# Optimization experiments

Measured on AMD Instinct MI355X. Metric: run time of the kernel, lower is better.

Reference implementation:

```python
import jax, jax.numpy as jnp
import numpy as np

B, T, D, K = 4, 2048, 1024, 4

def setup_inputs() -> dict:
    key = jax.random.key(0)
    ks = jax.random.split(key, 4)
    u = jax.random.normal(ks[0], (B, T, D), dtype=jnp.float32)
    s0 = jnp.zeros((B, K, D), dtype=jnp.float32)
    W_in = jax.random.normal(ks[1], (K * D, D), dtype=jnp.float32) * (1.0 / np.sqrt(D))
    b_in = jnp.zeros((K * D,), dtype=jnp.float32)
    W_out = jax.random.normal(ks[2], (D, K * D), dtype=jnp.float32) * (1.0 / np.sqrt(K * D))
    b_out = jnp.zeros((D,), dtype=jnp.float32)
    decay_logit = jax.random.normal(ks[3], (K,), dtype=jnp.float32)
    return {"u": u, "s0": s0, "W_in": W_in, "b_in": b_in,
            "W_out": W_out, "b_out": b_out, "decay_logit": decay_logit}

def reference(u, s0, W_in, b_in, W_out, b_out, decay_logit):
    # u: (B,T,D); s0: (B,K,D)
    Bb, Tt, Dd = u.shape
    Kk = decay_logit.shape[0]
    # input projection -> (B,T,K,D) -> (T,B,K,D) for scan over time
    inp = (jnp.einsum('btd,ed->bte', u, W_in) + b_in).reshape(Bb, Tt, Kk, Dd)
    xs = jnp.transpose(inp, (1, 0, 2, 3))  # (T,B,K,D)
    decay = jax.nn.sigmoid(decay_logit).reshape(1, Kk, 1)  # (1,K,1)

    def step(s, x):
        s_next = decay * s + x
        return s_next, s_next

    s_last, s_seq = jax.lax.scan(step, s0, xs)  # s_seq: (T,B,K,D)
    g_in = jnp.transpose(s_seq, (1, 0, 2, 3)).reshape(Bb, Tt, Kk * Dd)
    g = jnp.einsum('bte,de->btd', g_in, W_out) + b_out
    return g, s_last
```

## Files before the change

kernel.cpp:

```cpp
#include <hip/hip_runtime.h>


#define Bb 4
#define Tt 2048
#define Dd 1024
#define Kk 4
#define BT (Bb*Tt)
#define Ee (Kk*Dd)
#define NCH 32
#define LCH 64

typedef __bf16 bf16x8 __attribute__((ext_vector_type(8)));
typedef float  f32x4  __attribute__((ext_vector_type(4)));

__device__ __forceinline__ float bf2f(ushort u){
  union { unsigned int i; float f; } x; x.i = ((unsigned int)u) << 16; return x.f;
}
__device__ __forceinline__ ushort f2bf(float f){
  union { unsigned int i; float f; } x; x.f = f;
  unsigned int i = x.i;
  return (ushort)((i + 0x7FFFu + ((i >> 16) & 1u)) >> 16);
}
__device__ __forceinline__ float sigm(float x){ return 1.0f / (1.0f + expf(-x)); }

__global__ __launch_bounds__(256) void k_prep_all(
    const float* __restrict__ u, const float* __restrict__ dlog,
    float* __restrict__ vpart,
    const float* __restrict__ W_in, ushort* __restrict__ WinT,
    const float* __restrict__ Wout, const float* __restrict__ s0,
    const float* __restrict__ b_in, ushort* __restrict__ Wout_bf,
    float* __restrict__ z0, float* __restrict__ cterm){
  const int bid = blockIdx.x;
  const int tid = threadIdx.x;

  if (bid < 128){
    int x = bid, c = x & 31, b = x >> 5;
    int d0 = tid * 4;
    float p[4];
    #pragma unroll
    for (int k = 0; k < 4; ++k) p[k] = sigm(dlog[k]);
    f32x4 a0 = {0,0,0,0}, a1 = {0,0,0,0}, a2 = {0,0,0,0}, a3 = {0,0,0,0};
    size_t ub = ((size_t)(b*Tt + c*LCH)) * Dd + d0;
    for (int i = 0; i < LCH; ++i){
      f32x4 uv = *(const f32x4*)(u + ub);
      a0 = p[0]*a0 + uv; a1 = p[1]*a1 + uv; a2 = p[2]*a2 + uv; a3 = p[3]*a3 + uv;
      ub += Dd;
    }
    size_t vb = ((size_t)x * Kk) * Dd + d0;
    *(f32x4*)(vpart + vb)          = a0;
    *(f32x4*)(vpart + vb + Dd)     = a1;
    *(f32x4*)(vpart + vb + 2*Dd)   = a2;
    *(f32x4*)(vpart + vb + 3*Dd)   = a3;
  } else if (bid < 4224){
    __shared__ float tile[32][33];
    int bb = bid - 128;
    int c0 = (bb & 31) * 32, r0 = (bb >> 5) * 32;
    int tx = tid & 31, ty = tid >> 5;
    #pragma unroll
    for (int j = 0; j < 4; ++j)
      tile[ty + j*8][tx] = W_in[(size_t)(r0 + ty + j*8) * Dd + c0 + tx];
    __syncthreads();
    #pragma unroll
    for (int j = 0; j < 4; ++j)
      WinT[(size_t)(c0 + ty + j*8) * Ee + r0 + tx] = f2bf(tile[tx][ty + j*8]);
  } else {
    int gid  = (bid - 4224) * 4 + (tid >> 6);
    int lane = tid & 63;
    int d = gid & 1023, k = gid >> 10;
    const float* wrow = Wout + (size_t)d * Ee + k * Dd;
    ushort*      wbf  = Wout_bf + (size_t)d * Ee + k * Dd;
    const float* bv   = b_in + k * Dd;
    float sc = 0.f, sz0 = 0.f, sz1 = 0.f, sz2 = 0.f, sz3 = 0.f;
    #pragma unroll
    for (int j = 0; j < 4; ++j){
      int base = lane*4 + j*256;
      float4 wv = *(const float4*)(wrow + base);
      ushort4 ob; ob.x = f2bf(wv.x); ob.y = f2bf(wv.y); ob.z = f2bf(wv.z); ob.w = f2bf(wv.w);
      *(ushort4*)(wbf + base) = ob;
      float4 bb4 = *(const float4*)(bv + base);
      sc += wv.x*bb4.x + wv.y*bb4.y + wv.z*bb4.z + wv.w*bb4.w;
      #pragma unroll
      for (int b = 0; b < 4; ++b){
        const float* sv = s0 + ((size_t)(b*Kk + k) << 10) + base;
        float4 s4 = *(const float4*)sv;
        float acc = wv.x*s4.x + wv.y*s4.y + wv.z*s4.z + wv.w*s4.w;
        if (b == 0) sz0 += acc; else if (b == 1) sz1 += acc;
        else if (b == 2) sz2 += acc; else sz3 += acc;
      }
    }
    for (int off = 32; off; off >>= 1){
      sc  += __shfl_down(sc, off);
      sz0 += __shfl_down(sz0, off);
      sz1 += __shfl_down(sz1, off);
      sz2 += __shfl_down(sz2, off);
      sz3 += __shfl_down(sz3, off);
    }
    if (lane == 0){
      cterm[gid] = sc;
      z0[gid]          = sz0;
      z0[gid + 4096]   = sz1;
      z0[gid + 8192]   = sz2;
      z0[gid + 12288]  = sz3;
    }
  }
}

__global__ __launch_bounds__(256) void k_mid(const float* __restrict__ vpart,
                                             const float* __restrict__ dlog,
                                             float* __restrict__ incoming,
                                             float* __restrict__ vfull){
  int idx = blockIdx.x * 256 + threadIdx.x;
  int k = (idx >> 10) & 3, b = idx >> 12, d = idx & 1023;
  float p  = sigm(dlog[k]);
  float dL = powf(p, (float)LCH);
  float inc = 0.f;
  for (int c = 0; c < NCH; ++c){
    size_t o = (((size_t)(b*NCH + c)) * Kk + k) * Dd + d;
    incoming[o] = inc;
    inc = dL * inc + vpart[o];
  }
  vfull[idx] = inc;
}

__global__ __launch_bounds__(256) void k_zeta(const float* __restrict__ u,
                                              const float* __restrict__ incoming,
                                              const float* __restrict__ dlog,
                                              ushort* __restrict__ zeta){
  int x = blockIdx.x;
  int k = blockIdx.y;
  int c = x & 31, b = x >> 5;
  int d0 = threadIdx.x * 4;
  float p = sigm(dlog[k]);
  f32x4 z = *(const f32x4*)&incoming[(((size_t)x) * Kk + k) * Dd + d0];
  size_t ub = ((size_t)(b*Tt + c*LCH)) * Dd + d0;
  size_t zb = ((size_t)(b*Tt + c*LCH)) * Ee + k*Dd + d0;
  for (int i = 0; i < LCH; ++i){
    f32x4 uv = *(const f32x4*)(u + ub);
    z = p*z + uv;
    ushort4 o; o.x = f2bf(z[0]); o.y = f2bf(z[1]); o.z = f2bf(z[2]); o.w = f2bf(z[3]);
    *(ushort4*)(zeta + zb) = o;
    ub += Dd; zb += Ee;
  }
}

__global__ __launch_bounds__(256) void gemm_nt(const ushort* __restrict__ A,
                                               const ushort* __restrict__ B,
                                               ushort* __restrict__ C,
                                               int Kred, int lda, int ldb, int ldc,
                                               long aBatch, long bBatch, long cBatch){
  __shared__ ushort As[128 * 32];
  __shared__ ushort Bs[128 * 32];
  A += (long)blockIdx.z * aBatch;
  B += (long)blockIdx.z * bBatch;
  C += (long)blockIdx.z * cBatch;
  const int tid  = threadIdx.x;
  const int lane = tid & 63;
  const int w    = tid >> 6;
  const int wr   = w >> 1, wc = w & 1;
  const int rowBase = blockIdx.x * 128;
  const int colBase = blockIdx.y * 128;

  f32x4 acc[4][4] = {};
  const int krow = (lane >> 4) * 8;
  const int rsel = lane & 15;

  for (int kk = 0; kk < Kred; kk += 32){
    __syncthreads();
    #pragma unroll
    for (int i = 0; i < 2; ++i){
      int c  = i * 256 + tid;
      int r  = c >> 2;
      int c8 = (c & 3) * 8;
      const ushort* ga = A + (size_t)(rowBase + r) * lda + kk + c8;
      const ushort* gb = B + (size_t)(colBase + r) * ldb + kk + c8;
      __builtin_amdgcn_global_load_lds((const __attribute__((address_space(1))) void*)ga,
                                       (__attribute__((address_space(3))) void*)&As[c * 8],
                                       16, 0, 0);
      __builtin_amdgcn_global_load_lds((const __attribute__((address_space(1))) void*)gb,
                                       (__attribute__((address_space(3))) void*)&Bs[c * 8],
                                       16, 0, 0);
    }
    asm volatile("s_waitcnt vmcnt(0)" ::: "memory");
    __syncthreads();

    bf16x8 Af[4], Bf[4];
    #pragma unroll
    for (int mi = 0; mi < 4; ++mi)
      Af[mi] = *(const bf16x8*)&As[(wr*64 + mi*16 + rsel) * 32 + krow];
    #pragma unroll
    for (int ni = 0; ni < 4; ++ni)
      Bf[ni] = *(const bf16x8*)&Bs[(wc*64 + ni*16 + rsel) * 32 + krow];
    #pragma unroll
    for (int mi = 0; mi < 4; ++mi)
      #pragma unroll
      for (int ni = 0; ni < 4; ++ni)
        acc[mi][ni] = __builtin_amdgcn_mfma_f32_16x16x32_bf16(Af[mi], Bf[ni], acc[mi][ni], 0, 0, 0);
  }

  #pragma unroll
  for (int mi = 0; mi < 4; ++mi){
    #pragma unroll
    for (int ni = 0; ni < 4; ++ni){
      int r0 = rowBase + wr*64 + mi*16 + (lane >> 4) * 4;
      int c0 = colBase + wc*64 + ni*16 + (lane & 15);
      #pragma unroll
      for (int q = 0; q < 4; ++q)
        C[(size_t)(r0 + q) * ldc + c0] = f2bf(acc[mi][ni][q]);
    }
  }
}

#define STAGE_OP(GB, LOFF)                                                     \
  { _Pragma("unroll")                                                          \
    for (int i_ = 0; i_ < 2; ++i_){                                            \
      int c_ = tid + i_*256;                                                   \
      int row_ = c_ >> 2;                                                      \
      int ss_ = (c_ & 3) ^ ((row_ >> 1) & 3);                                  \
      const ushort* g_ = (GB) + (size_t)row_ * 4096 + ss_ * 8;                 \
      __builtin_amdgcn_global_load_lds(                                        \
        (const __attribute__((address_space(1))) void*)g_,                     \
        (__attribute__((address_space(3))) void*)&lds[(LOFF) + c_*8],          \
        16, 0, 0);                                                             \
    } }

#define LOAD_A4(DST)                                                           \
  { _Pragma("unroll")                                                          \
    for (int mi_ = 0; mi_ < 4; ++mi_){                                         \
      int r_ = wm*64 + mi_*16 + rsel;                                          \
      int uo_ = r_*32 + kq*8;                                                  \
      uo_ ^= ((uo_ >> 6) & 3) << 3;                                            \
      DST[mi_] = *(const bf16x8*)&lds[cbase + uo_];                            \
    } }

#define LOAD_B4(DST)                                                           \
  { _Pragma("unroll")                                                          \
    for (int ni_ = 0; ni_ < 4; ++ni_){                                         \
      int r_ = wn*64 + ni_*16 + rsel;                                          \
      int uo_ = r_*32 + kq*8;                                                  \
      uo_ ^= ((uo_ >> 6) & 3) << 3;                                            \
      DST[ni_] = *(const bf16x8*)&lds[cbase + 4096 + uo_];                     \
    } }

#define BAR() __builtin_amdgcn_s_barrier()

__global__ __launch_bounds__(256, 4) void gemm_big(const ushort* __restrict__ A,
                                                   const ushort* __restrict__ B,
                                                   float* __restrict__ g,
                                                   const float* __restrict__ dlog,
                                                   const float* __restrict__ z0,
                                                   const float* __restrict__ cterm,
                                                   const float* __restrict__ b_out){
  __shared__ ushort lds[16384];
  const int tid  = threadIdx.x;
  const int lane = tid & 63;
  const int w    = tid >> 6;
  const int wm   = w >> 1;
  const int wn   = w & 1;
  const int rsel = lane & 15;
  const int kq   = lane >> 4;

  int bid = blockIdx.x;
  int xcd = bid & 7, rr = bid >> 3;
  const int rowBase = (xcd * 8 + (rr & 7)) * 128;
  const int colBase = (rr >> 3) * 128;

  const ushort* Ag = A + (size_t)rowBase * 4096;
  const ushort* Bg = B + (size_t)colBase * 4096;

  f32x4 acc[4][4] = {};

  STAGE_OP(Ag +  0, 0);
  STAGE_OP(Bg +  0, 4096);
  STAGE_OP(Ag + 32, 8192);
  STAGE_OP(Bg + 32, 8192 + 4096);
  asm volatile("s_waitcnt vmcnt(4)" ::: "memory");
  BAR();

  for (int t = 0; t < 128; ++t){
    const int cbase = (t & 1) * 8192;
    bf16x8 af[4], bf[4];
    LOAD_A4(af); LOAD_B4(bf);
    #pragma unroll
    for (int mi = 0; mi < 4; ++mi)
      #pragma unroll
      for (int ni = 0; ni < 4; ++ni)
        acc[mi][ni] = __builtin_amdgcn_mfma_f32_16x16x32_bf16(af[mi], bf[ni], acc[mi][ni], 0, 0, 0);
    asm volatile("s_waitcnt lgkmcnt(0)" ::: "memory");
    BAR();
    if (t < 126){
      STAGE_OP(Ag + (t+2)*32, cbase);
      STAGE_OP(Bg + (t+2)*32, cbase + 4096);
      asm volatile("s_waitcnt vmcnt(4)" ::: "memory");
    } else {
      asm volatile("s_waitcnt vmcnt(0)" ::: "memory");
    }
    BAR();
  }

  {
    const int b  = rowBase >> 11;
    const int t0 = rowBase & 2047;
    const int c0 = colBase + wn*64 + rsel;
    float boj[4], ctsum[4], d0v[4][4];
    #pragma unroll
    for (int j = 0; j < 4; ++j){
      int cj = c0 + j*16;
      boj[j] = b_out[cj];
      float cs = 0.f;
      #pragma unroll
      for (int k = 0; k < 4; ++k){
        float p   = sigm(dlog[k]);
        float omp = fmaxf(1.0f - p, 1e-30f);
        float ct  = cterm[k*Dd + cj] / omp;
        d0v[k][j] = z0[b*4096 + k*Dd + cj] - ct;
        cs += ct;
      }
      ctsum[j] = cs;
    }
    float pk[4], p16[4], pwm[4];
    int tfirst = t0 + wm*64 + (lane >> 4)*4;
    #pragma unroll
    for (int k = 0; k < 4; ++k){
      pk[k]  = sigm(dlog[k]);
      pwm[k] = powf(pk[k], (float)(tfirst + 1));
      p16[k] = powf(pk[k], 16.0f);
    }
    #pragma unroll
    for (int mi = 0; mi < 4; ++mi){
      float pwr[4];
      #pragma unroll
      for (int k = 0; k < 4; ++k) pwr[k] = pwm[k];
      #pragma unroll
      for (int q = 0; q < 4; ++q){
        int r = rowBase + wm*64 + mi*16 + (lane >> 4)*4 + q;
        #pragma unroll
        for (int j = 0; j < 4; ++j){
          float gg = acc[mi][j][q] + boj[j] + ctsum[j];
          #pragma unroll
          for (int k = 0; k < 4; ++k) gg += pwr[k] * d0v[k][j];
          g[(size_t)r * Dd + c0 + j*16] = gg;
        }
        #pragma unroll
        for (int k = 0; k < 4; ++k) pwr[k] *= pk[k];
      }
      #pragma unroll
      for (int k = 0; k < 4; ++k) pwm[k] *= p16[k];
    }
  }
}

__global__ __launch_bounds__(256) void k_slast(const float* __restrict__ W_in,
                                               const float* __restrict__ vfull,
                                               const float* __restrict__ s0,
                                               const float* __restrict__ b_in,
                                               const float* __restrict__ dlog,
                                               float* __restrict__ out){
  int gid  = blockIdx.x * 4 + (threadIdx.x >> 6);
  int lane = threadIdx.x & 63;
  int d = gid & 1023, k = (gid >> 10) & 3, b = gid >> 12;
  const float* wrow = W_in + (size_t)(k*Dd + d) * Dd;
  const float* vv   = vfull + ((size_t)(b*Kk + k) << 10);
  float s = 0.f;
  #pragma unroll
  for (int j = 0; j < 4; ++j){
    int base = lane*4 + j*256;
    float4 w4 = *(const float4*)(wrow + base);
    float4 v4 = *(const float4*)(vv + base);
    s += w4.x*v4.x + w4.y*v4.y + w4.z*v4.z + w4.w*v4.w;
  }
  for (int off = 32; off; off >>= 1) s += __shfl_down(s, off);
  if (lane == 0){
    float p  = sigm(dlog[k]);
    float pT = powf(p, (float)Tt);
    float omp = 1.0f - p;
    float geo = (omp < 1e-12f) ? (float)Tt : (1.0f - pT) / omp;
    out[gid] = pT * s0[gid] + s + b_in[k*Dd + d] * geo;
  }
}

extern "C" void kernel_launch(void* const* d_in, const int* in_sizes, int n_in,
                              void* d_out, int out_size, void* d_ws, size_t ws_size,
                              hipStream_t stream){
  const float* u     = (const float*)d_in[0];
  const float* s0    = (const float*)d_in[1];
  const float* W_in  = (const float*)d_in[2];
  const float* b_in  = (const float*)d_in[3];
  const float* W_out = (const float*)d_in[4];
  const float* b_out = (const float*)d_in[5];
  const float* dlog  = (const float*)d_in[6];

  float* g_out     = (float*)d_out;
  float* slast_out = g_out + (size_t)BT * Dd;

  char* ws = (char*)d_ws;
  if (ws_size < 115490816ull) return;
  ushort* WinT    = (ushort*)(ws + 16777216);
  ushort* Wout_bf = (ushort*)(ws + 25165824);
  ushort* Mcat3   = (ushort*)(ws + 33554432);
  ushort* zeta    = (ushort*)(ws + 41943040);
  float*  incoming= (float*)(ws + 111149056);
  float*  z0buf   = (float*)(ws + 113246208);
  float*  cterm   = (float*)(ws + 113311744);
  float*  vpart   = (float*)(ws + 113328128);
  float*  vfull   = (float*)(ws + 115425280);

  k_prep_all<<<5248, 256, 0, stream>>>(u, dlog, vpart,
                                       W_in, WinT,
                                       W_out, s0, b_in, Wout_bf, z0buf, cterm);

  k_mid<<<64, 256, 0, stream>>>(vpart, dlog, incoming, vfull);

  k_zeta<<<dim3(128, 4), 256, 0, stream>>>(u, incoming, dlog, zeta);

  gemm_nt<<<dim3(8, 8, 4), 256, 0, stream>>>(Wout_bf, WinT, Mcat3,
                                             1024, Ee, Ee, Ee,
                                             1024L, 1024L, 1024L);

  gemm_big<<<512, 256, 0, stream>>>(zeta, Mcat3, g_out, dlog,
                                    z0buf, cterm, b_out);

  k_slast<<<4096, 256, 0, stream>>>(W_in, vfull, s0, b_in, dlog, slast_out);
}
```

Baseline: 158.0 us.

## Apply recurrence after GEMM on bf16 input instead of materializing zeta

Drops the zeta kernel, which wrote a BT×4096 bf16 scan of the input. The big GEMM now multiplies bf16 u (K=1024) against four per-k 1024×1024 fused matrices, and each block runs the per-k decay scan over the GEMM output in LDS, seeded by incoming-state projections computed in the block prologue. This cuts the reduction length of the main GEMM and removes a large intermediate write and read. In exchange it adds a serial 64-step scan per column inside the epilogue, a larger LDS footprint (512 threads, 2 blocks per CU), and bf16 rounding of the GEMM result before the scan.

Measured after the change: 319.5 us. +102.3%, slower.

```diff
diff --git a/kernel.cpp b/kernel.cpp
--- a/kernel.cpp
+++ b/kernel.cpp
@@ -25,7 +25,7 @@
 
 __global__ __launch_bounds__(256) void k_prep_all(
     const float* __restrict__ u, const float* __restrict__ dlog,
-    float* __restrict__ vpart,
+    float* __restrict__ vpart, ushort* __restrict__ U_bf,
     const float* __restrict__ W_in, ushort* __restrict__ WinT,
     const float* __restrict__ Wout, const float* __restrict__ s0,
     const float* __restrict__ b_in, ushort* __restrict__ Wout_bf,
@@ -43,6 +43,9 @@
     size_t ub = ((size_t)(b*Tt + c*LCH)) * Dd + d0;
     for (int i = 0; i < LCH; ++i){
       f32x4 uv = *(const f32x4*)(u + ub);
+      ushort4 ob; ob.x = f2bf(uv[0]); ob.y = f2bf(uv[1]);
+      ob.z = f2bf(uv[2]); ob.w = f2bf(uv[3]);
+      *(ushort4*)(U_bf + ub) = ob;
       a0 = p[0]*a0 + uv; a1 = p[1]*a1 + uv; a2 = p[2]*a2 + uv; a3 = p[3]*a3 + uv;
       ub += Dd;
     }
@@ -120,27 +123,6 @@
     inc = dL * inc + vpart[o];
   }
   vfull[idx] = inc;
-}
-
-__global__ __launch_bounds__(256) void k_zeta(const float* __restrict__ u,
-                                              const float* __restrict__ incoming,
-                                              const float* __restrict__ dlog,
-                                              ushort* __restrict__ zeta){
-  int x = blockIdx.x;
-  int k = blockIdx.y;
-  int c = x & 31, b = x >> 5;
-  int d0 = threadIdx.x * 4;
-  float p = sigm(dlog[k]);
-  f32x4 z = *(const f32x4*)&incoming[(((size_t)x) * Kk + k) * Dd + d0];
-  size_t ub = ((size_t)(b*Tt + c*LCH)) * Dd + d0;
-  size_t zb = ((size_t)(b*Tt + c*LCH)) * Ee + k*Dd + d0;
-  for (int i = 0; i < LCH; ++i){
-    f32x4 uv = *(const f32x4*)(u + ub);
-    z = p*z + uv;
-    ushort4 o; o.x = f2bf(z[0]); o.y = f2bf(z[1]); o.z = f2bf(z[2]); o.w = f2bf(z[3]);
-    *(ushort4*)(zeta + zb) = o;
-    ub += Dd; zb += Ee;
-  }
 }
 
 __global__ __launch_bounds__(256) void gemm_nt(const ushort* __restrict__ A,
@@ -210,52 +192,63 @@
   }
 }
 
-#define STAGE_OP(GB, LOFF)                                                     \
+#define GSTAGE_A(KK, LOFF)                                                     \
+  { int c_ = tid;                                                              \
+    int row_ = c_ >> 2;                                                        \
+    int ss_ = (c_ & 3) ^ ((row_ >> 1) & 3);                                    \
+    const ushort* g_ = U_bf + (size_t)(rowBase + row_) * 1024 + (KK) + ss_*8;  \
+    __builtin_amdgcn_global_load_lds(                                          \
+      (const __attribute__((address_space(1))) void*)g_,                       \
+      (__attribute__((address_space(3))) void*)&lds[(LOFF) + c_*8],            \
+      16, 0, 0); }
+
+#define GSTAGE_B(KK, LOFF)                                                     \
   { _Pragma("unroll")                                                          \
-    for (int i_ = 0; i_ < 2; ++i_){                                            \
-      int c_ = tid + i_*256;                                                   \
+    for (int s2_ = 0; s2_ < 4; ++s2_){                                         \
+      int c_ = tid;                                                            \
       int row_ = c_ >> 2;                                                      \
       int ss_ = (c_ & 3) ^ ((row_ >> 1) & 3);                                  \
-      const ushort* g_ = (GB) + (size_t)row_ * 4096 + ss_ * 8;                 \
+      const ushort* g_ = Mcat + (size_t)s2_*1048576                            \
+                       + (size_t)(colBase + row_) * 1024 + (KK) + ss_*8;       \
       __builtin_amdgcn_global_load_lds(                                        \
         (const __attribute__((address_space(1))) void*)g_,                     \
-        (__attribute__((address_space(3))) void*)&lds[(LOFF) + c_*8],          \
-        16, 0, 0);                                                             \
-    } }
-
-#define LOAD_A4(DST)                                                           \
+        (__attribute__((address_space(3))) void*)&lds[(LOFF) + 4096 + s2_*4096 + c_*8], \
+        16, 0, 0); } }
+
+#define GLOAD_A4(DST)                                                          \
   { _Pragma("unroll")                                                          \
     for (int mi_ = 0; mi_ < 4; ++mi_){                                         \
       int r_ = wm*64 + mi_*16 + rsel;                                          \
       int uo_ = r_*32 + kq*8;                                                  \
       uo_ ^= ((uo_ >> 6) & 3) << 3;                                            \
-      DST[mi_] = *(const bf16x8*)&lds[cbase + uo_];                            \
-    } }
-
-#define LOAD_B4(DST)                                                           \
+      DST[mi_] = *(const bf16x8*)&lds[cbase + uo_]; } }
+
+#define GLOAD_B8(DST)                                                          \
   { _Pragma("unroll")                                                          \
-    for (int ni_ = 0; ni_ < 4; ++ni_){                                         \
-      int r_ = wn*64 + ni_*16 + rsel;                                          \
+    for (int ni_ = 0; ni_ < 8; ++ni_){                                         \
+      int r_ = ni_*16 + rsel;                                                  \
       int uo_ = r_*32 + kq*8;                                                  \
       uo_ ^= ((uo_ >> 6) & 3) << 3;                                            \
-      DST[ni_] = *(const bf16x8*)&lds[cbase + 4096 + uo_];                     \
-    } }
+      DST[ni_] = *(const bf16x8*)&lds[cbase + 4096 + wn*4096 + uo_]; } }
 
 #define BAR() __builtin_amdgcn_s_barrier()
 
-__global__ __launch_bounds__(256, 4) void gemm_big(const ushort* __restrict__ A,
-                                                   const ushort* __restrict__ B,
-                                                   float* __restrict__ g,
-                                                   const float* __restrict__ dlog,
-                                                   const float* __restrict__ z0,
-                                                   const float* __restrict__ cterm,
-                                                   const float* __restrict__ b_out){
-  __shared__ ushort lds[16384];
+__global__ __launch_bounds__(512, 2) void gemm_g(const ushort* __restrict__ U_bf,
+                                                 const ushort* __restrict__ Mcat,
+                                                 const float* __restrict__ incoming,
+                                                 const float* __restrict__ dlog,
+                                                 const float* __restrict__ z0buf,
+                                                 const float* __restrict__ cterm,
+                                                 const float* __restrict__ b_out,
+                                                 float* __restrict__ g){
+  __shared__ ushort lds[67584];
+  float* gf    = (float*)&lds[32768];
+  float* incYf = (float*)&lds[65536];
   const int tid  = threadIdx.x;
   const int lane = tid & 63;
   const int w    = tid >> 6;
-  const int wm   = w >> 1;
-  const int wn   = w & 1;
+  const int wm   = w >> 2;
+  const int wn   = w & 3;
   const int rsel = lane & 15;
   const int kq   = lane >> 4;
 
@@ -263,89 +256,113 @@
   int xcd = bid & 7, rr = bid >> 3;
   const int rowBase = (xcd * 8 + (rr & 7)) * 128;
   const int colBase = (rr >> 3) * 128;
-
-  const ushort* Ag = A + (size_t)rowBase * 4096;
-  const ushort* Bg = B + (size_t)colBase * 4096;
-
-  f32x4 acc[4][4] = {};
-
-  STAGE_OP(Ag +  0, 0);
-  STAGE_OP(Bg +  0, 4096);
-  STAGE_OP(Ag + 32, 8192);
-  STAGE_OP(Bg + 32, 8192 + 4096);
-  asm volatile("s_waitcnt vmcnt(4)" ::: "memory");
+  const int b      = rowBase >> 11;
+  const int chunk0 = (rowBase & 2047) >> 6;
+  const int t0     = rowBase & 2047;
+
+  for (int task = tid; task < 1024; task += 512){
+    int dcol = task & 127, ch = (task >> 7) & 1, kk2 = task >> 8;
+    const ushort* mrow = Mcat + (size_t)kk2*1048576 + (size_t)(colBase + dcol)*1024;
+    const float*  iu   = incoming + (((size_t)(b*NCH + chunk0 + ch))*Kk + kk2)*Dd;
+    float s = 0.f;
+    for (int j = 0; j < 128; ++j){
+      bf16x8 m8 = *(const bf16x8*)(mrow + j*8);
+      f32x4 iA = *(const f32x4*)(iu + j*8);
+      f32x4 iB = *(const f32x4*)(iu + j*8 + 4);
+      s += (float)m8[0]*iA[0] + (float)m8[1]*iA[1] + (float)m8[2]*iA[2] + (float)m8[3]*iA[3]
+         + (float)m8[4]*iB[0] + (float)m8[5]*iB[1] + (float)m8[6]*iB[2] + (float)m8[7]*iB[3];
+    }
+    incYf[(kk2*2 + ch)*128 + dcol] = s;
+  }
+
+  f32x4 acc[4][8] = {};
+
+  GSTAGE_A(0, 0);      GSTAGE_B(0, 0);
+  GSTAGE_A(32, 20480); GSTAGE_B(32, 20480);
+  asm volatile("s_waitcnt vmcnt(5)" ::: "memory");
   BAR();
 
-  for (int t = 0; t < 128; ++t){
-    const int cbase = (t & 1) * 8192;
-    bf16x8 af[4], bf[4];
-    LOAD_A4(af); LOAD_B4(bf);
+  for (int t = 0; t < 32; ++t){
+    const int cbase = (t & 1) * 20480;
+    bf16x8 af[4], bfr[8];
+    GLOAD_A4(af); GLOAD_B8(bfr);
+    __builtin_amdgcn_s_setprio(1);
     #pragma unroll
     for (int mi = 0; mi < 4; ++mi)
       #pragma unroll
-      for (int ni = 0; ni < 4; ++ni)
-        acc[mi][ni] = __builtin_amdgcn_mfma_f32_16x16x32_bf16(af[mi], bf[ni], acc[mi][ni], 0, 0, 0);
+      for (int ni = 0; ni < 8; ++ni)
+        acc[mi][ni] = __builtin_amdgcn_mfma_f32_16x16x32_bf16(af[mi], bfr[ni], acc[mi][ni], 0, 0, 0);
+    __builtin_amdgcn_s_setprio(0);
     asm volatile("s_waitcnt lgkmcnt(0)" ::: "memory");
     BAR();
-    if (t < 126){
-      STAGE_OP(Ag + (t+2)*32, cbase);
-      STAGE_OP(Bg + (t+2)*32, cbase + 4096);
-      asm volatile("s_waitcnt vmcnt(4)" ::: "memory");
+    if (t < 30){
+      GSTAGE_A((t+2)*32, cbase);
+      GSTAGE_B((t+2)*32, cbase);
+      asm volatile("s_waitcnt vmcnt(5)" ::: "memory");
     } else {
       asm volatile("s_waitcnt vmcnt(0)" ::: "memory");
     }
     BAR();
   }
 
-  {
-    const int b  = rowBase >> 11;
-    const int t0 = rowBase & 2047;
-    const int c0 = colBase + wn*64 + rsel;
-    float boj[4], ctsum[4], d0v[4][4];
-    #pragma unroll
-    for (int j = 0; j < 4; ++j){
-      int cj = c0 + j*16;
-      boj[j] = b_out[cj];
-      float cs = 0.f;
+  #pragma unroll
+  for (int r = 0; r < 2; ++r){
+    BAR();
+    if ((wn >> 1) == r){
+      int kslot = wn & 1;
       #pragma unroll
-      for (int k = 0; k < 4; ++k){
-        float p   = sigm(dlog[k]);
-        float omp = fmaxf(1.0f - p, 1e-30f);
-        float ct  = cterm[k*Dd + cj] / omp;
-        d0v[k][j] = z0[b*4096 + k*Dd + cj] - ct;
-        cs += ct;
+      for (int mi = 0; mi < 4; ++mi)
+        #pragma unroll
+        for (int ni = 0; ni < 8; ++ni)
+          #pragma unroll
+          for (int q = 0; q < 4; ++q){
+            int row = wm*64 + mi*16 + (lane >> 4)*4 + q;
+            int col = ni*16 + rsel;
+            lds[kslot*16384 + row*128 + col] = f2bf(acc[mi][ni][q]);
+          }
+    }
+    BAR();
+    if (tid < 256){
+      int dcol = tid & 127, ch = tid >> 7;
+      int cj = colBase + dcol;
+      int ka = 2*r, kb2 = 2*r + 1;
+      float pa = sigm(dlog[ka]), pb = sigm(dlog[kb2]);
+      float za = incYf[(ka*2 + ch)*128 + dcol];
+      float zb = incYf[(kb2*2 + ch)*128 + dcol];
+      float cta = cterm[ka*1024 + cj]  / fmaxf(1.0f - pa, 1e-30f);
+      float ctb = cterm[kb2*1024 + cj] / fmaxf(1.0f - pb, 1e-30f);
+      float da = z0buf[b*4096 + ka*1024 + cj]  - cta;
+      float db = z0buf[b*4096 + kb2*1024 + cj] - ctb;
+      float e0 = (float)(t0 + ch*64 + 1);
+      float pwa = powf(pa, e0), pwb = powf(pb, e0);
+      float basev = 0.f;
+      if (r == 0){
+        basev = b_out[cj];
+        #pragma unroll
+        for (int k = 0; k < 4; ++k){
+          float pk = sigm(dlog[k]);
+          basev += cterm[k*1024 + cj] / fmaxf(1.0f - pk, 1e-30f);
+        }
       }
-      ctsum[j] = cs;
-    }
-    float pk[4], p16[4], pwm[4];
-    int tfirst = t0 + wm*64 + (lane >> 4)*4;
-    #pragma unroll
-    for (int k = 0; k < 4; ++k){
-      pk[k]  = sigm(dlog[k]);
-      pwm[k] = powf(pk[k], (float)(tfirst + 1));
-      p16[k] = powf(pk[k], 16.0f);
-    }
-    #pragma unroll
-    for (int mi = 0; mi < 4; ++mi){
-      float pwr[4];
-      #pragma unroll
-      for (int k = 0; k < 4; ++k) pwr[k] = pwm[k];
-      #pragma unroll
-      for (int q = 0; q < 4; ++q){
-        int r = rowBase + wm*64 + mi*16 + (lane >> 4)*4 + q;
-        #pragma unroll
-        for (int j = 0; j < 4; ++j){
-          float gg = acc[mi][j][q] + boj[j] + ctsum[j];
-          #pragma unroll
-          for (int k = 0; k < 4; ++k) gg += pwr[k] * d0v[k][j];
-          g[(size_t)r * Dd + c0 + j*16] = gg;
-        }
-        #pragma unroll
-        for (int k = 0; k < 4; ++k) pwr[k] *= pk[k];
+      for (int i = 0; i < 64; ++i){
+        int row = ch*64 + i;
+        za = pa*za + bf2f(lds[row*128 + dcol]);
+        zb = pb*zb + bf2f(lds[16384 + row*128 + dcol]);
+        float gv = za + zb + pwa*da + pwb*db + basev;
+        pwa *= pa; pwb *= pb;
+        if (r == 0) gf[row*128 + dcol]  = gv;
+        else        gf[row*128 + dcol] += gv;
       }
-      #pragma unroll
-      for (int k = 0; k < 4; ++k) pwm[k] *= p16[k];
-    }
+    }
+  }
+  BAR();
+
+  #pragma unroll
+  for (int j = 0; j < 8; ++j){
+    int idx = tid + j*512;
+    int rr_ = idx >> 5, cc = idx & 31;
+    *(f32x4*)&g[(size_t)(rowBase + rr_) * 1024 + colBase + cc*4] =
+        *(const f32x4*)&gf[rr_*128 + cc*4];
   }
 }
 
@@ -394,30 +411,28 @@
 
   char* ws = (char*)d_ws;
   if (ws_size < 115490816ull) return;
+  ushort* U_bf    = (ushort*)(ws);
   ushort* WinT    = (ushort*)(ws + 16777216);
   ushort* Wout_bf = (ushort*)(ws + 25165824);
-  ushort* Mcat3   = (ushort*)(ws + 33554432);
-  ushort* zeta    = (ushort*)(ws + 41943040);
+  ushort* Mcat    = (ushort*)(ws + 33554432);
   float*  incoming= (float*)(ws + 111149056);
   float*  z0buf   = (float*)(ws + 113246208);
   float*  cterm   = (float*)(ws + 113311744);
   float*  vpart   = (float*)(ws + 113328128);
   float*  vfull   = (float*)(ws + 115425280);
 
-  k_prep_all<<<5248, 256, 0, stream>>>(u, dlog, vpart,
+  k_prep_all<<<5248, 256, 0, stream>>>(u, dlog, vpart, U_bf,
                                        W_in, WinT,
                                        W_out, s0, b_in, Wout_bf, z0buf, cterm);
 
   k_mid<<<64, 256, 0, stream>>>(vpart, dlog, incoming, vfull);
 
-  k_zeta<<<dim3(128, 4), 256, 0, stream>>>(u, incoming, dlog, zeta);
-
-  gemm_nt<<<dim3(8, 8, 4), 256, 0, stream>>>(Wout_bf, WinT, Mcat3,
-                                             1024, Ee, Ee, Ee,
-                                             1024L, 1024L, 1024L);
-
-  gemm_big<<<512, 256, 0, stream>>>(zeta, Mcat3, g_out, dlog,
-                                    z0buf, cterm, b_out);
+  gemm_nt<<<dim3(8, 8, 4), 256, 0, stream>>>(Wout_bf, WinT, Mcat,
+                                             1024, Ee, Ee, Dd,
+                                             1024L, 1024L, 1048576L);
+
+  gemm_g<<<512, 512, 0, stream>>>(U_bf, Mcat, incoming, dlog,
+                                  z0buf, cterm, b_out, g_out);
 
   k_slast<<<4096, 256, 0, stream>>>(W_in, vfull, s0, b_in, dlog, slast_out);
 }
```
